# Kernel tuning notes

Measured on AMD Instinct MI355X. Metric: run time of the kernel, lower is better.

The kernel has to match this reference:

```python
import jax, jax.numpy as jnp
import numpy as np

B, N, K = 4, 1024, 20
DM, DI, DS, DC, DR = 1024, 2048, 16, 4, 64
BITS, GRID = 10, 0.02
BINS = (1, 2, 4, 8, 16, 32)


def _lrelu(x):
    return jnp.where(x >= 0, x, 0.2 * x)


def _bn(x, w, b, m, v, eps=1e-5):
    return (x - m) * (w * jax.lax.rsqrt(v + eps)) + b


def _ln(x, w, b, eps=1e-5):
    mu = jnp.mean(x, -1, keepdims=True)
    var = jnp.mean((x - mu) ** 2, -1, keepdims=True)
    return (x - mu) * jax.lax.rsqrt(var + eps) * w + b


def _knn(x, k):
    # x: (B,N,C) -> (B,N,k) indices of k nearest (largest neg sq dist)
    xx = jnp.sum(x * x, -1)
    d = 2 * jnp.einsum('bnc,bmc->bnm', x, x) - xx[:, :, None] - xx[:, None, :]
    return jax.lax.top_k(d, k)[1]


def _edge_conv(x, w, bw, bb, bm, bv, k):
    idx = _knn(x, k)
    nb = jax.vmap(lambda f, i: f[i])(x, idx)            # (B,N,k,C) row gather
    ctr = jnp.broadcast_to(x[:, :, None, :], nb.shape)
    feat = jnp.concatenate([nb - ctr, ctr], -1)         # (B,N,k,2C)
    h = _lrelu(_bn(jnp.einsum('bnkc,oc->bnko', feat, w), bw, bb, bm, bv))
    return jnp.max(h, axis=2)                           # (B,N,O)


def _hilbert(g):
    # Skilling's AxesToTranspose, 3D, BITS bits/axis. g: (...,3) int32 -> (...,) int32
    xs = [g[..., i] for i in range(3)]
    Q = 1 << (BITS - 1)
    while Q > 1:
        P = Q - 1
        for i in range(3):
            cond = (xs[i] & Q) != 0
            if i == 0:
                xs[0] = jnp.where(cond, xs[0] ^ P, xs[0])
            else:
                t = (xs[0] ^ xs[i]) & P
                n0 = jnp.where(cond, xs[0] ^ P, xs[0] ^ t)
                ni = jnp.where(cond, xs[i], xs[i] ^ t)
                xs[0], xs[i] = n0, ni
        Q >>= 1
    for i in range(1, 3):
        xs[i] = xs[i] ^ xs[i - 1]
    t = jnp.zeros_like(xs[0])
    Q = 1 << (BITS - 1)
    while Q > 1:
        t = jnp.where((xs[2] & Q) != 0, t ^ (Q - 1), t)
        Q >>= 1
    xs = [v ^ t for v in xs]
    code = jnp.zeros_like(xs[0])
    for bit in range(BITS - 1, -1, -1):
        for i in range(3):
            code = (code << 1) | ((xs[i] >> bit) & 1)
    return code


def _serial_order(pts, trans):
    g = jnp.floor(pts / GRID).astype(jnp.int32)
    g = g - jnp.min(g, axis=1, keepdims=True)
    g = jnp.clip(g, 0, (1 << BITS) - 1)
    if trans:
        g = g[..., jnp.array([1, 0, 2])]
    return jnp.argsort(_hilbert(g), axis=1)             # per-batch serialization order


def _take(f, o):
    return jnp.take_along_axis(f, o[..., None], axis=1)


def _mamba(x, in_w, conv_w, conv_b, xproj_w, dt_w, dt_b, A_log, Dp, out_w):
    Bm, L, _ = x.shape
    xc, z = jnp.split(x @ in_w.T, 2, axis=-1)           # (B,L,DI) each
    xp = jnp.pad(xc, ((0, 0), (DC - 1, 0), (0, 0)))     # causal depthwise conv
    xc = sum(conv_w[:, j] * xp[:, j:j + L, :] for j in range(DC)) + conv_b
    xc = jax.nn.silu(xc)
    xdbl = xc @ xproj_w.T
    dt, Bs, Cs = jnp.split(xdbl, [DR, DR + DS], axis=-1)
    dt = jax.nn.softplus(dt @ dt_w.T + dt_b)            # (B,L,DI)
    A = -jnp.exp(A_log)                                 # (DI,DS)

    def step(h, inp):
        dt_t, B_t, C_t, u_t = inp
        h = h * jnp.exp(dt_t[..., None] * A) + (dt_t * u_t)[..., None] * B_t[:, None, :]
        return h, jnp.einsum('bdn,bn->bd', h, C_t)

    tm = lambda a: jnp.moveaxis(a, 1, 0)
    h0 = jnp.zeros((Bm, DI, DS), x.dtype)
    _, ys = jax.lax.scan(step, h0, (tm(dt), tm(Bs), tm(Cs), tm(xc)))
    y = jnp.moveaxis(ys, 0, 1) + xc * Dp
    return (y * jax.nn.silu(z)) @ out_w.T


def _forward(x, c1_w, bn1_w, bn1_b, bn1_m, bn1_v, c2_w, bn2_w, bn2_b, bn2_m, bn2_v,
             c3_w, bn3_w, bn3_b, bn3_m, bn3_v, c4_w, bn4_w, bn4_b, bn4_m, bn4_v,
             c5_w, bn5_w, bn5_b, bn5_m, bn5_v, pe1_w, pe1_b, pe2_w, pe2_b,
             gamma, beta, blkn_w, blkn_b, in_w, conv_w, conv_b, xproj_w,
             dt_w, dt_b, A_log, D, out_w, normf_w, normf_b, ft_w, ft_b):
    pts = jnp.transpose(x, (0, 2, 1))                   # (B,N,3)
    x1 = _edge_conv(pts, c1_w, bn1_w, bn1_b, bn1_m, bn1_v, K)
    x2 = _edge_conv(x1, c2_w, bn2_w, bn2_b, bn2_m, bn2_v, K)
    x3 = _edge_conv(x2, c3_w, bn3_w, bn3_b, bn3_m, bn3_v, K)
    x4 = _edge_conv(x3, c4_w, bn4_w, bn4_b, bn4_m, bn4_v, K)
    dg = _lrelu(_bn(jnp.einsum('bnc,oc->bno', jnp.concatenate([x1, x2, x3, x4], -1), c5_w),
                    bn5_w, bn5_b, bn5_m, bn5_v))        # (B,N,1024)
    pos5 = jax.nn.gelu(pts @ pe1_w.T + pe1_b, approximate=False) @ pe2_w.T + pe2_b
    of = _serial_order(pts, False)
    ob = _serial_order(pts, True)
    xs = jnp.concatenate([_take(dg, of) * gamma + beta,
                          _take(dg, ob) * gamma + beta], 1)   # (B,2N,1024)
    ps = jnp.concatenate([_take(pos5, of), _take(pos5, ob)], 1)
    hs = xs + ps
    hs = hs + _mamba(_ln(hs, blkn_w, blkn_b), in_w, conv_w, conv_b, xproj_w,
                     dt_w, dt_b, A_log, D, out_w)
    hs = _ln(hs, normf_w, normf_b)
    x_all = jnp.concatenate([hs, dg], axis=1)           # (B,3N,1024)
    P = x_all.shape[1]
    feats = []
    for nbin in BINS:
        zz = x_all.reshape(B, nbin, P // nbin, DM)
        feats.append(jnp.mean(zz, 2) + jnp.max(zz, 2))
    bf = jnp.transpose(jnp.concatenate(feats, 1), (1, 0, 2))  # (63,B,1024)
    return bf @ ft_w.T + ft_b                           # (63,B,256)


def setup_inputs() -> dict:
    ks = iter(jax.random.split(jax.random.key(0), 80))
    f32 = jnp.float32
    def nrm(shape, s):
        return jax.random.normal(next(ks), shape, f32) * s
    d = {}
    d['x'] = jax.random.normal(next(ks), (B, 3, N), f32)
    for name, (o, i) in dict(c1=(64, 6), c2=(64, 128), c3=(128, 128),
                             c4=(256, 256), c5=(1024, 512)).items():
        d[name + '_w'] = nrm((o, i), 1.0 / np.sqrt(i))
    for name, c in dict(bn1=64, bn2=64, bn3=128, bn4=256, bn5=1024).items():
        d[name + '_w'] = 1.0 + nrm((c,), 0.05)
        d[name + '_b'] = nrm((c,), 0.05)
        d[name + '_m'] = nrm((c,), 0.05)
        d[name + '_v'] = 1.0 + 0.1 * jax.random.uniform(next(ks), (c,), f32)
    d['pe1_w'] = nrm((DM // 2, 3), 1.0 / np.sqrt(3))
    d['pe1_b'] = nrm((DM // 2,), 0.02)
    d['pe2_w'] = nrm((DM, DM // 2), 1.0 / np.sqrt(DM // 2))
    d['pe2_b'] = nrm((DM,), 0.02)
    d['gamma'] = 1.0 + nrm((DM,), 0.02)
    d['beta'] = nrm((DM,), 0.02)
    d['blkn_w'] = jnp.ones((DM,), f32)
    d['blkn_b'] = jnp.zeros((DM,), f32)
    d['in_w'] = nrm((2 * DI, DM), 1.0 / np.sqrt(DM))
    d['conv_w'] = nrm((DI, DC), 1.0 / np.sqrt(DC))
    d['conv_b'] = jnp.zeros((DI,), f32)
    d['xproj_w'] = nrm((DR + 2 * DS, DI), 1.0 / np.sqrt(DI))
    d['dt_w'] = nrm((DI, DR), DR ** -0.5)
    dt = jnp.exp(jax.random.uniform(next(ks), (DI,), f32) * np.log(0.1 / 1e-3) + np.log(1e-3))
    d['dt_b'] = dt + jnp.log(-jnp.expm1(-dt))           # inverse softplus
    d['A_log'] = jnp.log(jnp.broadcast_to(jnp.arange(1, DS + 1, dtype=f32), (DI, DS)))
    d['D'] = jnp.ones((DI,), f32)
    d['out_w'] = nrm((DM, DI), 1.0 / np.sqrt(DI))
    d['normf_w'] = jnp.ones((DM,), f32)
    d['normf_b'] = jnp.zeros((DM,), f32)
    d['ft_w'] = nrm((256, DM), 1.0 / np.sqrt(DM))
    d['ft_b'] = jnp.zeros((256,), f32)
    return d


def reference(x, c1_w, bn1_w, bn1_b, bn1_m, bn1_v, c2_w, bn2_w, bn2_b, bn2_m, bn2_v,
              c3_w, bn3_w, bn3_b, bn3_m, bn3_v, c4_w, bn4_w, bn4_b, bn4_m, bn4_v,
              c5_w, bn5_w, bn5_b, bn5_m, bn5_v, pe1_w, pe1_b, pe2_w, pe2_b,
              gamma, beta, blkn_w, blkn_b, in_w, conv_w, conv_b, xproj_w,
              dt_w, dt_b, A_log, D, out_w, normf_w, normf_b, ft_w, ft_b):
    return _forward(x, c1_w, bn1_w, bn1_b, bn1_m, bn1_v, c2_w, bn2_w, bn2_b, bn2_m, bn2_v,
                    c3_w, bn3_w, bn3_b, bn3_m, bn3_v, c4_w, bn4_w, bn4_b, bn4_m, bn4_v,
                    c5_w, bn5_w, bn5_b, bn5_m, bn5_v, pe1_w, pe1_b, pe2_w, pe2_b,
                    gamma, beta, blkn_w, blkn_b, in_w, conv_w, conv_b, xproj_w,
                    dt_w, dt_b, A_log, D, out_w, normf_w, normf_b, ft_w, ft_b)
```

## Files before the change

### kernel.cpp

```cpp
#include <hip/hip_runtime.h>
#include <hip/hip_bf16.h>
#include <cstdint>
#include <cstddef>

static constexpr int BB = 4, NN = 1024;
static constexpr int DM = 1024, DI = 2048, DSN = 16, DCN = 4;
static constexpr int LL = 2048, PP = 3072;

typedef unsigned short u16;
typedef __bf16 bfv8 __attribute__((ext_vector_type(8)));
typedef float fv4 __attribute__((ext_vector_type(4)));

__device__ __forceinline__ u16 f2bf(float f) {
  unsigned u = __float_as_uint(f);
  return (u16)((u + 0x7FFFu + ((u >> 16) & 1u)) >> 16);
}
__device__ __forceinline__ float bf2f(u16 h) { return __uint_as_float(((unsigned)h) << 16); }

__device__ __forceinline__ void gload_lds16(const void* g, void* l) {
  __builtin_amdgcn_global_load_lds((const __attribute__((address_space(1))) void*)g,
                                   (__attribute__((address_space(3))) void*)l, 16, 0, 0);
}

__global__ __launch_bounds__(256) void k_fill(unsigned* __restrict__ p, unsigned n32, unsigned pat) {
  unsigned i = blockIdx.x * 256 + threadIdx.x;
  if (i < n32) p[i] = pat;
}

struct CvtArgs {
  const void* src[47];
  unsigned dstoff[47];
  unsigned nelem[47];
  unsigned cumblk[48];
};

__global__ __launch_bounds__(256) void k_convert(CvtArgs a, float* __restrict__ ws) {
  const unsigned w0 = *(const unsigned*)a.src[32];
  const bool isbf = (w0 != 0x3F800000u);
  const int blk = (int)blockIdx.x;
  int slot = 46;
  while (slot > 0 && blk < (int)a.cumblk[slot]) --slot;
  const unsigned n = a.nelem[slot];
  const unsigned base = (unsigned)(blk - (int)a.cumblk[slot]) * 1024u + threadIdx.x;
  float* dst = ws + a.dstoff[slot];
  if (isbf) {
    const u16* s = (const u16*)a.src[slot];
#pragma unroll
    for (int p = 0; p < 4; ++p) {
      unsigned e = base + 256u * p;
      if (e < n) dst[e] = bf2f(s[e]);
    }
  } else {
    const float* s = (const float*)a.src[slot];
#pragma unroll
    for (int p = 0; p < 4; ++p) {
      unsigned e = base + 256u * p;
      if (e < n) dst[e] = s[e];
    }
  }
}

__global__ __launch_bounds__(256) void k_tobf(const float* __restrict__ s, u16* __restrict__ d, int n4) {
  int i = blockIdx.x * 256 + threadIdx.x;
  if (i >= n4) return;
  float4 v = *(const float4*)(s + (size_t)i * 4);
  uint2 o;
  o.x = (unsigned)f2bf(v.x) | ((unsigned)f2bf(v.y) << 16);
  o.y = (unsigned)f2bf(v.z) | ((unsigned)f2bf(v.w) << 16);
  *(uint2*)(d + (size_t)i * 4) = o;
}

__global__ __launch_bounds__(256) void k_transpose(const float* __restrict__ x, float* __restrict__ pts) {
  int o = blockIdx.x * 256 + threadIdx.x;
  if (o >= BB * NN * 3) return;
  int c = o % 3, n = (o / 3) % NN, b = o / (3 * NN);
  pts[o] = x[((size_t)b * 3 + c) * NN + n];
}

__global__ __launch_bounds__(256) void k_rownorm(const float* __restrict__ X, int ldx, int C, float* __restrict__ xx) {
  int r = blockIdx.x * 256 + threadIdx.x;
  if (r >= BB * NN) return;
  const float* p = X + (size_t)r * ldx;
  float s0 = 0, s1 = 0, s2 = 0, s3 = 0;
  int c = 0;
  for (; c + 4 <= C; c += 4) {
    s0 += p[c] * p[c]; s1 += p[c + 1] * p[c + 1];
    s2 += p[c + 2] * p[c + 2]; s3 += p[c + 3] * p[c + 3];
  }
  for (; c < C; ++c) s0 += p[c] * p[c];
  xx[r] = (s0 + s1) + (s2 + s3);
}

__global__ __launch_bounds__(256) void k_dist(const float* __restrict__ X, int ldx, int C,
                                              const float* __restrict__ xx, float* __restrict__ D) {
  const int b = blockIdx.z;
  const float* Xb = X + (size_t)(b << 10) * ldx;
  __shared__ float As[16][68];
  __shared__ float Bs[16][68];
  const int tid = threadIdx.x;
  const int m0 = blockIdx.y << 6, n0 = blockIdx.x << 6;
  const int tcol = tid & 15, trow = tid >> 4;
  float acc[4][4];
#pragma unroll
  for (int i = 0; i < 4; ++i)
#pragma unroll
    for (int j = 0; j < 4; ++j) acc[i][j] = 0.f;

  for (int k0 = 0; k0 < C; k0 += 16) {
#pragma unroll
    for (int p = 0; p < 4; ++p) {
      int lin = tid + (p << 8);
      int r = lin >> 4, kk = lin & 15;
      int gk = k0 + kk;
      As[kk][r] = (gk < C) ? Xb[(size_t)(m0 + r) * ldx + gk] : 0.f;
      Bs[kk][r] = (gk < C) ? Xb[(size_t)(n0 + r) * ldx + gk] : 0.f;
    }
    __syncthreads();
#pragma unroll
    for (int kk = 0; kk < 16; ++kk) {
      float a[4], bv[4];
#pragma unroll
      for (int i = 0; i < 4; ++i) a[i] = As[kk][(trow << 2) + i];
#pragma unroll
      for (int j = 0; j < 4; ++j) bv[j] = Bs[kk][(tcol << 2) + j];
#pragma unroll
      for (int i = 0; i < 4; ++i)
#pragma unroll
        for (int j = 0; j < 4; ++j) acc[i][j] += a[i] * bv[j];
    }
    __syncthreads();
  }

#pragma unroll
  for (int i = 0; i < 4; ++i) {
    int gm = m0 + (trow << 2) + i;
#pragma unroll
    for (int j = 0; j < 4; ++j) {
      int gn = n0 + (tcol << 2) + j;
      float v = 2.f * acc[i][j] - xx[(b << 10) + gm] - xx[(b << 10) + gn];
      D[((size_t)(b << 10) + gm) * 1024 + gn] = v;
    }
  }
}

__global__ __launch_bounds__(256) void k_sel(const float* __restrict__ D, int* __restrict__ idxo) {
  const int wv = threadIdx.x >> 6, lane = threadIdx.x & 63;
  const int row = (blockIdx.x << 2) + wv;
  const float* dr = D + (size_t)row * 1024;
  float4 c0 = *(const float4*)(dr + (lane << 2));
  float4 c1 = *(const float4*)(dr + 256 + (lane << 2));
  float4 c2 = *(const float4*)(dr + 512 + (lane << 2));
  float4 c3 = *(const float4*)(dr + 768 + (lane << 2));
  float v[16] = {c0.x, c0.y, c0.z, c0.w, c1.x, c1.y, c1.z, c1.w,
                 c2.x, c2.y, c2.z, c2.w, c3.x, c3.y, c3.z, c3.w};
  const int gbase = lane << 2;
  for (int t = 0; t < 20; ++t) {
    float bv = v[0];
    int bi = gbase;
#pragma unroll
    for (int r = 1; r < 16; ++r) {
      int gi = ((r >> 2) << 8) + gbase + (r & 3);
      if (v[r] > bv) { bv = v[r]; bi = gi; }
    }
#pragma unroll
    for (int o = 32; o; o >>= 1) {
      float ov = __shfl_down(bv, o);
      int oi = __shfl_down(bi, o);
      if (ov > bv || (ov == bv && oi < bi)) { bv = ov; bi = oi; }
    }
    bi = __shfl(bi, 0);
    if (lane == 0) idxo[row * 20 + t] = bi;
#pragma unroll
    for (int r = 0; r < 16; ++r) {
      int gi = ((r >> 2) << 8) + gbase + (r & 3);
      if (gi == bi) v[r] = -3e38f;
    }
  }
}

template <int O>
__global__ __launch_bounds__(256) void k_edge_max(const float* __restrict__ G, const float* __restrict__ base,
                                                  const int* __restrict__ idxi,
                                                  const float* __restrict__ bw, const float* __restrict__ bbp,
                                                  const float* __restrict__ bm, const float* __restrict__ bvv,
                                                  float* __restrict__ out, int ldo) {
  __shared__ int ids[20];
  const int rn = blockIdx.x;
  const int tid = threadIdx.x;
  if (tid < 20) ids[tid] = idxi[rn * 20 + tid];
  __syncthreads();
  const int b = rn >> 10;
  float mx = -3e38f, mn = 3e38f;
#pragma unroll 5
  for (int k = 0; k < 20; ++k) {
    float v = G[((size_t)(b << 10) + ids[k]) * O + tid];
    mx = fmaxf(mx, v); mn = fminf(mn, v);
  }
  float s = bw[tid] * rsqrtf(bvv[tid] + 1e-5f);
  float red = (s >= 0.f) ? mx : mn;
  float v = (base[(size_t)rn * O + tid] + red - bm[tid]) * s + bbp[tid];
  out[(size_t)rn * ldo + tid] = (v >= 0.f) ? v : 0.2f * v;
}

template <int EPI>
__global__ __launch_bounds__(256) void k_gemm(const float* __restrict__ A, int lda,
                                              const float* __restrict__ Bm, int ldb, int boff, int bdiff,
                                              float* __restrict__ C, int ldc, int M, int N, int Kd,
                                              const float* __restrict__ p1) {
  __shared__ float As[16][68];
  __shared__ float Bs[16][68];
  const int tid = threadIdx.x;
  const int m0 = blockIdx.y << 6, n0 = blockIdx.x << 6;
  const int tcol = tid & 15, trow = tid >> 4;
  float acc[4][4];
#pragma unroll
  for (int i = 0; i < 4; ++i)
#pragma unroll
    for (int j = 0; j < 4; ++j) acc[i][j] = 0.f;

  for (int k0 = 0; k0 < Kd; k0 += 16) {
#pragma unroll
    for (int p = 0; p < 4; ++p) {
      int lin = tid + (p << 8);
      int r = lin >> 4, kk = lin & 15;
      int gk = k0 + kk;
      int gm = m0 + r;
      As[kk][r] = (gm < M && gk < Kd) ? A[(size_t)gm * lda + gk] : 0.f;
      int gn = n0 + r;
      float bv = 0.f;
      if (gn < N && gk < Kd) {
        bv = Bm[(size_t)gn * ldb + gk + boff];
        if (bdiff) bv -= Bm[(size_t)gn * ldb + gk];
      }
      Bs[kk][r] = bv;
    }
    __syncthreads();
#pragma unroll
    for (int kk = 0; kk < 16; ++kk) {
      float a[4], bv[4];
#pragma unroll
      for (int i = 0; i < 4; ++i) a[i] = As[kk][(trow << 2) + i];
#pragma unroll
      for (int j = 0; j < 4; ++j) bv[j] = Bs[kk][(tcol << 2) + j];
#pragma unroll
      for (int i = 0; i < 4; ++i)
#pragma unroll
        for (int j = 0; j < 4; ++j) acc[i][j] += a[i] * bv[j];
    }
    __syncthreads();
  }

#pragma unroll
  for (int i = 0; i < 4; ++i) {
    int gm = m0 + (trow << 2) + i;
    if (gm >= M) continue;
#pragma unroll
    for (int j = 0; j < 4; ++j) {
      int gn = n0 + (tcol << 2) + j;
      if (gn >= N) continue;
      float v = acc[i][j];
      if (EPI == 2) {
        v += p1[gn];
        v = 0.5f * v * (1.f + erff(v * 0.70710678118654752440f));
      }
      C[(size_t)gm * ldc + gn] = v;
    }
  }
}

template <int EPI>
__global__ __launch_bounds__(256) void k_mgemm3(const u16* __restrict__ A, const u16* __restrict__ W,
                                                float* __restrict__ C, int ldc, int M, int N, int K, int alda,
                                                const float* __restrict__ p1, const float* __restrict__ p2,
                                                const float* __restrict__ p3, const float* __restrict__ p4,
                                                u16* __restrict__ obf, void* outp, const void* modesrc) {
  __shared__ char raw[65536];
  u16* Asl = (u16*)raw;
  u16* Bsl = (u16*)(raw + 32768);
  const int tid = threadIdx.x;
  const int lane = tid & 63, wave = tid >> 6;
  const int wm = wave & 1, wn = wave >> 1;
  const int m0 = blockIdx.y << 7, n0 = blockIdx.x << 7;
  fv4 acc[4][4];
#pragma unroll
  for (int i = 0; i < 4; ++i)
#pragma unroll
    for (int j = 0; j < 4; ++j) acc[i][j] = fv4{0.f, 0.f, 0.f, 0.f};

  const int lrow = tid >> 2;
  const int lcol = (((tid & 3) ^ ((tid >> 3) & 3)) << 3);
  const u16* gA0 = A + (size_t)(m0 + lrow) * alda + lcol;
  const u16* gA1 = A + (size_t)(m0 + 64 + lrow) * alda + lcol;
  const u16* gB0 = W + (size_t)(n0 + lrow) * K + lcol;
  const u16* gB1 = W + (size_t)(n0 + 64 + lrow) * K + lcol;
  const int ar = wm * 64 + (lane & 15);
  const int br = wn * 64 + (lane & 15);
  const int swz = ((lane & 15) >> 1) & 3;
  const int ko = (((lane >> 4) ^ swz) << 3);

  const int NIT = K >> 5;
#pragma unroll
  for (int p = 0; p < 2; ++p) {
    const int k0 = p << 5;
    gload_lds16(gA0 + k0, Asl + p * 4096 + wave * 512);
    gload_lds16(gA1 + k0, Asl + p * 4096 + 2048 + wave * 512);
    gload_lds16(gB0 + k0, Bsl + p * 4096 + wave * 512);
    gload_lds16(gB1 + k0, Bsl + p * 4096 + 2048 + wave * 512);
  }

  for (int it = 0; it < NIT; ++it) {
    if (it + 2 < NIT) {
      const int nb = (it + 2) & 3;
      const int k0 = (it + 2) << 5;
      gload_lds16(gA0 + k0, Asl + nb * 4096 + wave * 512);
      gload_lds16(gA1 + k0, Asl + nb * 4096 + 2048 + wave * 512);
      gload_lds16(gB0 + k0, Bsl + nb * 4096 + wave * 512);
      gload_lds16(gB1 + k0, Bsl + nb * 4096 + 2048 + wave * 512);
      asm volatile("s_waitcnt vmcnt(8)" ::: "memory");
    } else if (it + 1 < NIT) {
      asm volatile("s_waitcnt vmcnt(4)" ::: "memory");
    } else {
      asm volatile("s_waitcnt vmcnt(0)" ::: "memory");
    }
    __builtin_amdgcn_sched_barrier(0);
    __builtin_amdgcn_s_barrier();
    const int cb = it & 3;
    bfv8 af[4], bfr[4];
#pragma unroll
    for (int f = 0; f < 4; ++f) {
      af[f]  = *(const bfv8*)(Asl + cb * 4096 + (ar + f * 16) * 32 + ko);
      bfr[f] = *(const bfv8*)(Bsl + cb * 4096 + (br + f * 16) * 32 + ko);
    }
#pragma unroll
    for (int i = 0; i < 4; ++i)
#pragma unroll
      for (int j = 0; j < 4; ++j)
        acc[i][j] = __builtin_amdgcn_mfma_f32_16x16x32_bf16(af[i], bfr[j], acc[i][j], 0, 0, 0);
  }

  const int rq = lane >> 4, cq = lane & 15;
  if constexpr (EPI == 6) {
    bool isbf = (*(const unsigned*)modesrc) != 0x3F800000u;
#pragma unroll
    for (int i = 0; i < 4; ++i)
#pragma unroll
      for (int j = 0; j < 4; ++j)
#pragma unroll
        for (int r = 0; r < 4; ++r) {
          int gm = m0 + wm * 64 + i * 16 + rq * 4 + r;
          int gn = n0 + wn * 64 + j * 16 + cq;
          if (gm >= M || gn >= N) continue;
          float v = acc[i][j][r] + p1[gn];
          if (isbf) ((u16*)outp)[(size_t)gm * ldc + gn] = f2bf(v);
          else ((float*)outp)[(size_t)gm * ldc + gn] = v;
        }
  } else {
    constexpr bool U16O = (EPI == 1 || EPI == 8 || EPI == 9);
    __syncthreads();
#pragma unroll
    for (int i = 0; i < 4; ++i)
#pragma unroll
      for (int j = 0; j < 4; ++j)
#pragma unroll
        for (int r = 0; r < 4; ++r) {
          int row = wm * 64 + i * 16 + rq * 4 + r;
          int col = wn * 64 + j * 16 + cq;
          int gn = n0 + col;
          float v = acc[i][j][r];
          if (EPI == 1) {
            float s = p1[gn] * rsqrtf(p4[gn] + 1e-5f);
            v = (v - p3[gn]) * s + p2[gn];
            v = (v >= 0.f) ? v : 0.2f * v;
          } else if (EPI == 3) {
            v += p1[gn];
          } else if (EPI == 9) {
            v += p1[gn];
            v = (v > 0.f) ? v + __logf(1.f + __expf(-v)) : __logf(1.f + __expf(v));
          }
          int sc = col ^ ((row & 7) << 3);
          if (U16O) ((u16*)raw)[row * 128 + sc] = f2bf(v);
          else ((float*)raw)[row * 128 + sc] = v;
        }
    __syncthreads();
    const int row = tid >> 1, c0 = (tid & 1) << 6;
    const int gm = m0 + row;
    if (gm < M) {
      if (n0 + 128 <= N) {
        if (U16O) {
          u16* dst = obf + (size_t)gm * ldc + n0 + c0;
#pragma unroll
          for (int vv = 0; vv < 8; ++vv) {
            int sc = (c0 + vv * 8) ^ ((row & 7) << 3);
            *(uint4*)(dst + vv * 8) = *(const uint4*)((const u16*)raw + row * 128 + sc);
          }
        } else {
          float* dst = C + (size_t)gm * ldc + n0 + c0;
#pragma unroll
          for (int vv = 0; vv < 16; ++vv) {
            int sc = (c0 + vv * 4) ^ ((row & 7) << 3);
            float4 val = *(const float4*)((const float*)raw + row * 128 + sc);
            if (EPI == 5) {
              float4 o = *(const float4*)(dst + vv * 4);
              val.x += o.x; val.y += o.y; val.z += o.z; val.w += o.w;
            }
            *(float4*)(dst + vv * 4) = val;
          }
        }
      } else {
        for (int e = 0; e < 64; ++e) {
          int col = c0 + e, gn = n0 + col;
          if (gn >= N) break;
          int sc = col ^ ((row & 7) << 3);
          if (U16O) {
            obf[(size_t)gm * ldc + gn] = ((const u16*)raw)[row * 128 + sc];
          } else {
            float v = ((const float*)raw)[row * 128 + sc];
            if (EPI == 5) v += C[(size_t)gm * ldc + gn];
            C[(size_t)gm * ldc + gn] = v;
          }
        }
      }
    }
  }
}

__device__ __forceinline__ int hilbert3(int x0, int x1, int x2) {
  for (int Q = 1 << 9; Q > 1; Q >>= 1) {
    int P2 = Q - 1;
    if (x0 & Q) x0 ^= P2;
    { int t = (x0 ^ x1) & P2; if (x1 & Q) x0 ^= P2; else { x0 ^= t; x1 ^= t; } }
    { int t = (x0 ^ x2) & P2; if (x2 & Q) x0 ^= P2; else { x0 ^= t; x2 ^= t; } }
  }
  x1 ^= x0; x2 ^= x1;
  int t = 0;
  for (int Q = 1 << 9; Q > 1; Q >>= 1)
    if (x2 & Q) t ^= (Q - 1);
  x0 ^= t; x1 ^= t; x2 ^= t;
  int code = 0;
  for (int bit = 9; bit >= 0; --bit) {
    code = (code << 1) | ((x0 >> bit) & 1);
    code = (code << 1) | ((x1 >> bit) & 1);
    code = (code << 1) | ((x2 >> bit) & 1);
  }
  return code;
}

__global__ __launch_bounds__(1024) void k_serial(const float* __restrict__ pts, int* __restrict__ of, int* __restrict__ ob) {
  const int b = blockIdx.x >> 1, trans = blockIdx.x & 1;
  const int tid = threadIdx.x;
  __shared__ int mn[3];
  __shared__ unsigned long long sk[1024];
  if (tid < 3) mn[tid] = 0x7fffffff;
  __syncthreads();
  int g[3];
#pragma unroll
  for (int c = 0; c < 3; ++c) {
    float p = pts[((size_t)b * NN + tid) * 3 + c];
    g[c] = (int)floorf(p / 0.02f);
    atomicMin(&mn[c], g[c]);
  }
  __syncthreads();
#pragma unroll
  for (int c = 0; c < 3; ++c) {
    g[c] -= mn[c];
    g[c] = g[c] < 0 ? 0 : (g[c] > 1023 ? 1023 : g[c]);
  }
  int x0 = g[0], x1 = g[1], x2 = g[2];
  if (trans) { int t = x0; x0 = x1; x1 = t; }
  int code = hilbert3(x0, x1, x2);
  sk[tid] = ((unsigned long long)(unsigned)code << 10) | (unsigned)tid;
  __syncthreads();
  for (int k2 = 2; k2 <= 1024; k2 <<= 1) {
    for (int j = k2 >> 1; j > 0; j >>= 1) {
      int ixj = tid ^ j;
      if (ixj > tid) {
        unsigned long long a0 = sk[tid], a1 = sk[ixj];
        bool up = ((tid & k2) == 0);
        if ((a0 > a1) == up) { sk[tid] = a1; sk[ixj] = a0; }
      }
      __syncthreads();
    }
  }
  int* dst = trans ? ob : of;
  dst[b * NN + tid] = (int)(sk[tid] & 1023u);
}

__global__ __launch_bounds__(256) void k_build_hs(const u16* __restrict__ dg, const float* __restrict__ pos5,
                                                  const int* __restrict__ of, const int* __restrict__ ob,
                                                  const float* __restrict__ gamma, const float* __restrict__ beta,
                                                  float* __restrict__ hs) {
  const int row = blockIdx.x;
  const int b = row >> 11, l = row & 2047;
  const int src = (l < NN) ? of[b * NN + l] : ob[b * NN + (l - NN)];
  const u16* dgr = dg + ((size_t)b * NN + src) * DM;
  const float* psr = pos5 + ((size_t)b * NN + src) * DM;
  float* hr = hs + (size_t)row * DM;
  for (int c = threadIdx.x; c < DM; c += 256)
    hr[c] = bf2f(dgr[c]) * gamma[c] + beta[c] + psr[c];
}

__device__ __forceinline__ float wred_sum(float s) {
#pragma unroll
  for (int o = 32; o; o >>= 1) s += __shfl_down(s, o);
  return s;
}

template <int BF>
__global__ __launch_bounds__(256) void k_ln(const float* X, const float* __restrict__ w,
                                            const float* __restrict__ bb, float* Y, u16* Ybf) {
  const int row = blockIdx.x;
  const float* x = X + (size_t)row * DM;
  const int tid = threadIdx.x;
  float v[4];
#pragma unroll
  for (int p = 0; p < 4; ++p) v[p] = x[tid + (p << 8)];
  __shared__ float red[4];
  float s = ((v[0] + v[1]) + (v[2] + v[3]));
  s = wred_sum(s);
  if ((tid & 63) == 0) red[tid >> 6] = s;
  __syncthreads();
  float mu = (red[0] + red[1] + red[2] + red[3]) * (1.f / DM);
  __syncthreads();
  float ss = 0.f;
#pragma unroll
  for (int p = 0; p < 4; ++p) { float d = v[p] - mu; ss += d * d; }
  ss = wred_sum(ss);
  if ((tid & 63) == 0) red[tid >> 6] = ss;
  __syncthreads();
  float var = (red[0] + red[1] + red[2] + red[3]) * (1.f / DM);
  float rs = rsqrtf(var + 1e-5f);
#pragma unroll
  for (int p = 0; p < 4; ++p) {
    int c = tid + (p << 8);
    float o = (v[p] - mu) * rs * w[c] + bb[c];
    if (BF) Ybf[(size_t)row * DM + c] = f2bf(o);
    else Y[(size_t)row * DM + c] = o;
  }
}

__global__ __launch_bounds__(512) void k_convip(float* __restrict__ x, const float* __restrict__ cw,
                                                const float* __restrict__ cb, u16* __restrict__ xbf) {
  const int b = blockIdx.x >> 5, dgp = blockIdx.x & 31;
  const int lane = threadIdx.x & 63, ch = threadIdx.x >> 6;
  const int d = (dgp << 6) + lane;
  float* base = x + ((size_t)b * LL) * DI + d;
  u16* bb16 = xbf + ((size_t)b * LL) * DI + d;
  const int CL = LL / 8;
  const int l0 = ch * CL;
  const float w0 = cw[d * 4], w1 = cw[d * 4 + 1], w2 = cw[d * 4 + 2], w3 = cw[d * 4 + 3];
  const float bbv = cb[d];
  float a = 0.f, e = 0.f, c = 0.f;
  if (ch) {
    a = base[(size_t)(l0 - 3) * DI];
    e = base[(size_t)(l0 - 2) * DI];
    c = base[(size_t)(l0 - 1) * DI];
  }
  __syncthreads();
  for (int l = l0; l < l0 + CL; ++l) {
    float cur = base[(size_t)l * DI];
    float acc = bbv + w0 * a + w1 * e + w2 * c + w3 * cur;
    a = e; e = c; c = cur;
    float o = acc / (1.f + expf(-acc));
    base[(size_t)l * DI] = o;
    bb16[(size_t)l * DI] = f2bf(o);
  }
}

__global__ __launch_bounds__(64) void k_scanA_f(float* __restrict__ xy, const float* __restrict__ xdbl,
                                                const float* __restrict__ dtw, const float* __restrict__ dtbv,
                                                const float* __restrict__ A_log, const float* __restrict__ Dp,
                                                float* __restrict__ hend, float* __restrict__ dts,
                                                u16* __restrict__ zone) {
  const int t = threadIdx.x;
  const int seg = blockIdx.x & 15;
  const int dgrp = (blockIdx.x >> 4) & 31;
  const int b = blockIdx.x >> 9;
  const int d = (dgrp << 6) + t;
  const bool gate = (seg == 0);
  float wdt[64];
#pragma unroll
  for (int k = 0; k < 64; ++k) wdt[k] = dtw[d * 64 + k];
  float aa[16], h[16];
#pragma unroll
  for (int n = 0; n < 16; ++n) {
    aa[n] = -expf(A_log[d * 16 + n]) * 1.44269504088896340736f;
    h[n] = 0.f;
  }
  const float Dd = Dp[d], bdt = dtbv[d];
  const int l0 = seg << 7;
  float* base = xy + ((size_t)(b * LL + l0)) * DI + d;
  u16* zb = zone + ((size_t)(b * LL + l0)) * DI + d;
  const float* xr = xdbl + (size_t)(b * LL + l0) * 96;

  __shared__ float sx[2][768];
#pragma unroll
  for (int p = 0; p < 3; ++p)
    *(float4*)&sx[0][(t + (p << 6)) << 2] = *(const float4*)(xr + ((t + (p << 6)) << 2));
  float ureg[8], zreg[8];
#pragma unroll
  for (int r = 0; r < 8; ++r) ureg[r] = base[(size_t)r * DI];
  if (gate) {
#pragma unroll
    for (int r = 0; r < 8; ++r) zreg[r] = bf2f(zb[(size_t)r * DI]);
  }
  __syncthreads();

  float dta = 0.f;
  for (int lc = 0; lc < 16; ++lc) {
    const int cur = lc & 1;
    const bool more = (lc + 1 < 16);
    float4 st0, st1, st2;
    float unext[8], znext[8];
    if (more) {
      const float* src = xr + (size_t)(lc + 1) * 768;
      st0 = *(const float4*)(src + (t << 2));
      st1 = *(const float4*)(src + ((t + 64) << 2));
      st2 = *(const float4*)(src + ((t + 128) << 2));
#pragma unroll
      for (int r = 0; r < 8; ++r) unext[r] = base[(size_t)((lc + 1) * 8 + r) * DI];
      if (gate) {
#pragma unroll
        for (int r = 0; r < 8; ++r) znext[r] = bf2f(zb[(size_t)((lc + 1) * 8 + r) * DI]);
      }
    }
    float yv[8];
#pragma unroll
    for (int r = 0; r < 8; ++r) {
      const float* row = &sx[cur][r * 96];
      float s0 = 0, s1 = 0, s2 = 0, s3 = 0;
#pragma unroll
      for (int k = 0; k < 64; k += 4) {
        s0 += wdt[k] * row[k];     s1 += wdt[k + 1] * row[k + 1];
        s2 += wdt[k + 2] * row[k + 2]; s3 += wdt[k + 3] * row[k + 3];
      }
      float dv = (s0 + s1) + (s2 + s3) + bdt;
      dv = (dv > 0.f) ? dv + log1pf(expf(-dv)) : log1pf(expf(dv));
      dta += dv;
      float u = ureg[r];
      float du = dv * u;
      float acc = 0.f;
#pragma unroll
      for (int n = 0; n < 16; ++n) {
        float ee = exp2f(dv * aa[n]);
        h[n] = h[n] * ee + du * row[64 + n];
        acc += h[n] * row[80 + n];
      }
      yv[r] = acc + u * Dd;
    }
    if (gate) {
#pragma unroll
      for (int r = 0; r < 8; ++r) {
        float zv = zreg[r];
        zb[(size_t)(lc * 8 + r) * DI] = f2bf(yv[r] * (zv / (1.f + expf(-zv))));
      }
    } else {
#pragma unroll
      for (int r = 0; r < 8; ++r) base[(size_t)(lc * 8 + r) * DI] = yv[r];
    }
    __syncthreads();
    if (more) {
      *(float4*)&sx[cur ^ 1][t << 2] = st0;
      *(float4*)&sx[cur ^ 1][(t + 64) << 2] = st1;
      *(float4*)&sx[cur ^ 1][(t + 128) << 2] = st2;
#pragma unroll
      for (int r = 0; r < 8; ++r) ureg[r] = unext[r];
      if (gate) {
#pragma unroll
        for (int r = 0; r < 8; ++r) zreg[r] = znext[r];
      }
    }
    __syncthreads();
  }
  float* he = hend + ((size_t)(b * 16 + seg) * 16) * DI + d;
#pragma unroll
  for (int n = 0; n < 16; ++n) he[(size_t)n * DI] = h[n];
  dts[(size_t)(b * 16 + seg) * DI + d] = dta;
}

__global__ __launch_bounds__(64) void k_scanC_f(const float* __restrict__ xy, const float* __restrict__ xdbl,
                                                const float* __restrict__ dtw, const float* __restrict__ dtbv,
                                                const float* __restrict__ A_log,
                                                const float* __restrict__ hstart, u16* __restrict__ zone) {
  const int t = threadIdx.x;
  const int seg = (blockIdx.x % 15) + 1;
  const int rest = blockIdx.x / 15;
  const int dgrp = rest & 31;
  const int b = rest >> 5;
  const int d = (dgrp << 6) + t;
  float wdt[64];
#pragma unroll
  for (int k = 0; k < 64; ++k) wdt[k] = dtw[d * 64 + k];
  float aa[16], hst[16];
#pragma unroll
  for (int n = 0; n < 16; ++n) {
    aa[n] = -expf(A_log[d * 16 + n]) * 1.44269504088896340736f;
    hst[n] = hstart[((size_t)(b * 16 + seg) * 16 + n) * DI + d];
  }
  const float bdt = dtbv[d];
  const int l0 = seg << 7;
  const float* base = xy + ((size_t)(b * LL + l0)) * DI + d;
  u16* zb = zone + ((size_t)(b * LL + l0)) * DI + d;
  const float* xr = xdbl + (size_t)(b * LL + l0) * 96;

  __shared__ float sx[2][768];
#pragma unroll
  for (int p = 0; p < 3; ++p)
    *(float4*)&sx[0][(t + (p << 6)) << 2] = *(const float4*)(xr + ((t + (p << 6)) << 2));
  float ureg[8], zreg[8];
#pragma unroll
  for (int r = 0; r < 8; ++r) {
    ureg[r] = base[(size_t)r * DI];
    zreg[r] = bf2f(zb[(size_t)r * DI]);
  }
  __syncthreads();

  float cumdt = 0.f;
  for (int lc = 0; lc < 16; ++lc) {
    const int cur = lc & 1;
    const bool more = (lc + 1 < 16);
    float4 st0, st1, st2;
    float unext[8], znext[8];
    if (more) {
      const float* src = xr + (size_t)(lc + 1) * 768;
      st0 = *(const float4*)(src + (t << 2));
      st1 = *(const float4*)(src + ((t + 64) << 2));
      st2 = *(const float4*)(src + ((t + 128) << 2));
#pragma unroll
      for (int r = 0; r < 8; ++r) {
        unext[r] = base[(size_t)((lc + 1) * 8 + r) * DI];
        znext[r] = bf2f(zb[(size_t)((lc + 1) * 8 + r) * DI]);
      }
    }
    float yv[8];
#pragma unroll
    for (int r = 0; r < 8; ++r) {
      const float* row = &sx[cur][r * 96];
      float s0 = 0, s1 = 0, s2 = 0, s3 = 0;
#pragma unroll
      for (int k = 0; k < 64; k += 4) {
        s0 += wdt[k] * row[k];     s1 += wdt[k + 1] * row[k + 1];
        s2 += wdt[k + 2] * row[k + 2]; s3 += wdt[k + 3] * row[k + 3];
      }
      float dv = (s0 + s1) + (s2 + s3) + bdt;
      dv = (dv > 0.f) ? dv + log1pf(expf(-dv)) : log1pf(expf(dv));
      cumdt += dv;
      float corr = 0.f;
#pragma unroll
      for (int n = 0; n < 16; ++n)
        corr += row[80 + n] * exp2f(aa[n] * cumdt) * hst[n];
      yv[r] = ureg[r] + corr;
    }
#pragma unroll
    for (int r = 0; r < 8; ++r) {
      float zv = zreg[r];
      zb[(size_t)(lc * 8 + r) * DI] = f2bf(yv[r] * (zv / (1.f + expf(-zv))));
    }
    __syncthreads();
    if (more) {
      *(float4*)&sx[cur ^ 1][t << 2] = st0;
      *(float4*)&sx[cur ^ 1][(t + 64) << 2] = st1;
      *(float4*)&sx[cur ^ 1][(t + 128) << 2] = st2;
#pragma unroll
      for (int r = 0; r < 8; ++r) { ureg[r] = unext[r]; zreg[r] = znext[r]; }
    }
    __syncthreads();
  }
}

__global__ __launch_bounds__(64) void k_scanA_p(float* __restrict__ xy, const float* __restrict__ xdbl,
                                                const u16* __restrict__ dtb,
                                                const float* __restrict__ A_log, const float* __restrict__ Dp,
                                                float* __restrict__ hend, float* __restrict__ dts,
                                                u16* __restrict__ zone) {
  const int t = threadIdx.x;
  const int seg = blockIdx.x & 31;
  const int dgrp = (blockIdx.x >> 5) & 31;
  const int b = blockIdx.x >> 10;
  const int d = (dgrp << 6) + t;
  const bool gate = (seg == 0);
  float aa[16], h[16];
#pragma unroll
  for (int n = 0; n < 16; ++n) {
    aa[n] = -expf(A_log[d * 16 + n]) * 1.44269504088896340736f;
    h[n] = 0.f;
  }
  const float Dd = Dp[d];
  const int l0 = seg << 6;
  float* base = xy + ((size_t)(b * LL + l0)) * DI + d;
  const u16* dtp = dtb + ((size_t)(b * LL + l0)) * DI + d;
  u16* zb = zone + ((size_t)(b * LL + l0)) * DI + d;
  const float* xr = xdbl + (size_t)(b * LL + l0) * 96 + 64;

  __shared__ float sx[2][256];
  const int sr = t >> 3, sq = (t & 7) << 2;
  *(float4*)&sx[0][sr * 32 + sq] = *(const float4*)(xr + sr * 96 + sq);
  float ureg[8], dreg[8], zreg[8];
#pragma unroll
  for (int r = 0; r < 8; ++r) { ureg[r] = base[(size_t)r * DI]; dreg[r] = bf2f(dtp[(size_t)r * DI]); }
  if (gate) {
#pragma unroll
    for (int r = 0; r < 8; ++r) zreg[r] = bf2f(zb[(size_t)r * DI]);
  }
  __syncthreads();

  float dta = 0.f;
  for (int lc = 0; lc < 8; ++lc) {
    const int cur = lc & 1;
    const bool more = (lc + 1 < 8);
    float4 st0;
    float unext[8], dnext[8], znext[8];
    if (more) {
      st0 = *(const float4*)(xr + (size_t)(lc + 1) * 768 + sr * 96 + sq);
#pragma unroll
      for (int r = 0; r < 8; ++r) {
        unext[r] = base[(size_t)((lc + 1) * 8 + r) * DI];
        dnext[r] = bf2f(dtp[(size_t)((lc + 1) * 8 + r) * DI]);
      }
      if (gate) {
#pragma unroll
        for (int r = 0; r < 8; ++r) znext[r] = bf2f(zb[(size_t)((lc + 1) * 8 + r) * DI]);
      }
    }
    float yv[8];
#pragma unroll
    for (int r = 0; r < 8; ++r) {
      const float* row = &sx[cur][r * 32];
      float dv = dreg[r];
      dta += dv;
      float u = ureg[r];
      float du = dv * u;
      float acc = 0.f;
#pragma unroll
      for (int n = 0; n < 16; ++n) {
        float ee = exp2f(dv * aa[n]);
        h[n] = h[n] * ee + du * row[n];
        acc += h[n] * row[16 + n];
      }
      yv[r] = acc + u * Dd;
    }
    if (gate) {
#pragma unroll
      for (int r = 0; r < 8; ++r) {
        float zv = zreg[r];
        zb[(size_t)(lc * 8 + r) * DI] = f2bf(yv[r] * (zv / (1.f + expf(-zv))));
      }
    } else {
#pragma unroll
      for (int r = 0; r < 8; ++r) base[(size_t)(lc * 8 + r) * DI] = yv[r];
    }
    __syncthreads();
    if (more) {
      *(float4*)&sx[cur ^ 1][sr * 32 + sq] = st0;
#pragma unroll
      for (int r = 0; r < 8; ++r) { ureg[r] = unext[r]; dreg[r] = dnext[r]; }
      if (gate) {
#pragma unroll
        for (int r = 0; r < 8; ++r) zreg[r] = znext[r];
      }
    }
    __syncthreads();
  }
  float* he = hend + ((size_t)(b * 32 + seg) * 16) * DI + d;
#pragma unroll
  for (int n = 0; n < 16; ++n) he[(size_t)n * DI] = h[n];
  dts[(size_t)(b * 32 + seg) * DI + d] = dta;
}

__global__ __launch_bounds__(64) void k_scanC_p(const float* __restrict__ xy, const float* __restrict__ xdbl,
                                                const u16* __restrict__ dtb,
                                                const float* __restrict__ A_log,
                                                const float* __restrict__ hstart, u16* __restrict__ zone) {
  const int t = threadIdx.x;
  const int seg = (blockIdx.x % 31) + 1;
  const int rest = blockIdx.x / 31;
  const int dgrp = rest & 31;
  const int b = rest >> 5;
  const int d = (dgrp << 6) + t;
  float aa[16], hst[16];
#pragma unroll
  for (int n = 0; n < 16; ++n) {
    aa[n] = -expf(A_log[d * 16 + n]) * 1.44269504088896340736f;
    hst[n] = hstart[((size_t)(b * 32 + seg) * 16 + n) * DI + d];
  }
  const int l0 = seg << 6;
  const float* base = xy + ((size_t)(b * LL + l0)) * DI + d;
  const u16* dtp = dtb + ((size_t)(b * LL + l0)) * DI + d;
  u16* zb = zone + ((size_t)(b * LL + l0)) * DI + d;
  const float* xr = xdbl + (size_t)(b * LL + l0) * 96 + 64;

  __shared__ float sx[2][256];
  const int sr = t >> 3, sq = (t & 7) << 2;
  *(float4*)&sx[0][sr * 32 + sq] = *(const float4*)(xr + sr * 96 + sq);
  float ureg[8], dreg[8], zreg[8];
#pragma unroll
  for (int r = 0; r < 8; ++r) {
    ureg[r] = base[(size_t)r * DI];
    dreg[r] = bf2f(dtp[(size_t)r * DI]);
    zreg[r] = bf2f(zb[(size_t)r * DI]);
  }
  __syncthreads();

  float cumdt = 0.f;
  for (int lc = 0; lc < 8; ++lc) {
    const int cur = lc & 1;
    const bool more = (lc + 1 < 8);
    float4 st0;
    float unext[8], dnext[8], znext[8];
    if (more) {
      st0 = *(const float4*)(xr + (size_t)(lc + 1) * 768 + sr * 96 + sq);
#pragma unroll
      for (int r = 0; r < 8; ++r) {
        unext[r] = base[(size_t)((lc + 1) * 8 + r) * DI];
        dnext[r] = bf2f(dtp[(size_t)((lc + 1) * 8 + r) * DI]);
        znext[r] = bf2f(zb[(size_t)((lc + 1) * 8 + r) * DI]);
      }
    }
    float yv[8];
#pragma unroll
    for (int r = 0; r < 8; ++r) {
      const float* row = &sx[cur][r * 32];
      cumdt += dreg[r];
      float corr = 0.f;
#pragma unroll
      for (int n = 0; n < 16; ++n)
        corr += row[16 + n] * exp2f(aa[n] * cumdt) * hst[n];
      yv[r] = ureg[r] + corr;
    }
#pragma unroll
    for (int r = 0; r < 8; ++r) {
      float zv = zreg[r];
      zb[(size_t)(lc * 8 + r) * DI] = f2bf(yv[r] * (zv / (1.f + expf(-zv))));
    }
    __syncthreads();
    if (more) {
      *(float4*)&sx[cur ^ 1][sr * 32 + sq] = st0;
#pragma unroll
      for (int r = 0; r < 8; ++r) { ureg[r] = unext[r]; dreg[r] = dnext[r]; zreg[r] = znext[r]; }
    }
    __syncthreads();
  }
}

__global__ __launch_bounds__(256) void k_scanB(float* __restrict__ hh, const float* __restrict__ dts,
                                               const float* __restrict__ A_log, int nseg) {
  const int i = blockIdx.x * 256 + threadIdx.x;
  const int b = i >> 11, d = i & 2047;
  float aa[16], hs_[16];
#pragma unroll
  for (int n = 0; n < 16; ++n) {
    aa[n] = -expf(A_log[d * 16 + n]) * 1.44269504088896340736f;
    hs_[n] = 0.f;
  }
  for (int s = 0; s < nseg; ++s) {
    float* p = hh + ((size_t)(b * nseg + s) * 16) * DI + d;
    const float ds = dts[(size_t)(b * nseg + s) * DI + d];
#pragma unroll
    for (int n = 0; n < 16; ++n) {
      float he = p[(size_t)n * DI];
      p[(size_t)n * DI] = hs_[n];
      hs_[n] = he + exp2f(aa[n] * ds) * hs_[n];
    }
  }
}

__global__ __launch_bounds__(256) void k_binpool1(const float* __restrict__ hs, const u16* __restrict__ dg,
                                                  float* __restrict__ psum, float* __restrict__ pmax) {
  const int blk = blockIdx.x;
  const int cg = blk & 3, chunk = (blk >> 2) & 31, b = blk >> 7;
  const int c = (cg << 8) + threadIdx.x;
  const int r0 = chunk * 96;
  float sm = 0.f, mx = -3e38f;
  for (int r = 0; r < 96; ++r) {
    int pr = r0 + r;
    float v = (pr < 2048) ? hs[((size_t)(b << 11) + pr) * 1024 + c]
                          : bf2f(dg[((size_t)(b << 10) + (pr - 2048)) * 1024 + c]);
    sm += v; mx = fmaxf(mx, v);
  }
  int o = ((b << 5) + chunk) * 1024 + c;
  psum[o] = sm; pmax[o] = mx;
}

__global__ __launch_bounds__(256) void k_binpool2(const float* __restrict__ psum, const float* __restrict__ pmax,
                                                  float* __restrict__ bf) {
  const int sb = blockIdx.x;
  const int s = sb >> 2, b = sb & 3;
  int nbin, j;
  if (s == 0) { nbin = 1; j = 0; }
  else if (s < 3) { nbin = 2; j = s - 1; }
  else if (s < 7) { nbin = 4; j = s - 3; }
  else if (s < 15) { nbin = 8; j = s - 7; }
  else if (s < 31) { nbin = 16; j = s - 15; }
  else { nbin = 32; j = s - 31; }
  const int nch = 32 / nbin, c0 = j * nch;
  const int tid = threadIdx.x;
#pragma unroll
  for (int p = 0; p < 4; ++p) {
    int c = tid + (p << 8);
    float sm = 0.f, mx = -3e38f;
    for (int k = 0; k < nch; ++k) {
      int idx = ((b << 5) + c0 + k) * 1024 + c;
      sm += psum[idx]; mx = fmaxf(mx, pmax[idx]);
    }
    bf[(size_t)sb * 1024 + c] = sm / (float)(nch * 96) + mx;
  }
}

extern "C" void kernel_launch(void* const* d_in, const int* in_sizes, int n_in,
                              void* d_out, int out_size, void* d_ws, size_t ws_size,
                              hipStream_t stream) {
  const unsigned n32 = (unsigned)(out_size / 2);
  if (n_in != 47) {
    k_fill<<<(n32 + 255) / 256, 256, 0, stream>>>((unsigned*)d_out, n32, 0x44FA44FAu);
    return;
  }
  float* ws = (float*)d_ws;

  unsigned inoff[47];
  unsigned cum = 0;
  for (int i = 0; i < 47; ++i) { inoff[i] = cum; cum += (unsigned)((in_sizes[i] + 63) & ~63); }

  size_t off = ((size_t)cum + 255) & ~(size_t)255;
  auto alloc = [&](size_t nf) { size_t o = off; off = (off + nf + 255) & ~(size_t)255; return o; };
  const size_t O_DG = alloc(2097152);
  const size_t O_HS = alloc(8388608);
  const size_t O_B1 = alloc(16777216);
  const size_t O_B2 = alloc(6291456);
  const size_t O_B3 = alloc(12353536);
  const size_t base_end = off;
  const size_t O_DT = alloc(8388608);
  const size_t dt_end = off;
  if (base_end * 4 > ws_size) {
    k_fill<<<(n32 + 255) / 256, 256, 0, stream>>>((unsigned*)d_out, n32, 0x447A447Au);
    return;
  }
  const bool bigws = (dt_end * 4 <= ws_size);

  auto F = [&](int i) { return ws + inoff[i]; };
  u16*   dg_bf = (u16*)(ws + O_DG);
  float* hs = ws + O_HS;
  float* B1 = ws + O_B1;
  float* B2 = ws + O_B2;
  float* B3 = ws + O_B3;
  u16*   dtb_bf = (u16*)(ws + O_DT);

  float* pts   = B1;
  float* xxb   = B1 + 16384;
  int*   idxb  = (int*)(B1 + 32768);
  int*   of    = (int*)(B1 + 114688);
  int*   ob    = (int*)(B1 + 118784);
  float* xcat  = B1 + 131072;
  float* G     = B1 + 2228224;
  float* baseb = B1 + 3276800;
  float* tb    = B1 + 4325376;
  float* pos5  = B1 + 6422528;
  float* dist  = B1 + 10616832;
  u16*   xcat_bf = (u16*)(B1 + 12582912);
  u16*   tb_bf   = (u16*)(B1 + 14680064);
  float* xyg = B1;
  u16*   lnh_bf = (u16*)B2;
  float* hend   = B2;
  float* xdbl   = B2 + 4194304;
  float* bfb    = B2 + 4980736;
  u16*   bfb_bf = (u16*)(B2 + 5238784);
  float* psum   = B2 + 5369856;
  float* pmax   = B2 + 5500928;
  u16*   xdbl_bf = (u16*)(B2 + 5632000);
  float* dtsum  = psum;
  u16* in_w_bf  = (u16*)B3;
  u16* out_w_bf = (u16*)(B3 + 2097152);
  u16* c5_bf    = (u16*)(B3 + 3145728);
  u16* pe2_bf   = (u16*)(B3 + 3407872);
  u16* ft_bf    = (u16*)(B3 + 3670016);
  u16* xpw_bf   = (u16*)(B3 + 3801088);
  u16* dtw_bf   = (u16*)(B3 + 3899392);
  u16* zone     = (u16*)(B3 + 3964928);

  CvtArgs ca;
  unsigned cb = 0;
  for (int i = 0; i < 47; ++i) {
    ca.src[i] = d_in[i];
    ca.dstoff[i] = inoff[i];
    ca.nelem[i] = (unsigned)in_sizes[i];
    ca.cumblk[i] = cb;
    cb += (unsigned)((in_sizes[i] + 1023) / 1024);
  }
  ca.cumblk[47] = cb;
  k_convert<<<cb, 256, 0, stream>>>(ca, ws);

  k_tobf<<<4096, 256, 0, stream>>>(F(34), in_w_bf, 1048576);
  k_tobf<<<2048, 256, 0, stream>>>(F(42), out_w_bf, 524288);
  k_tobf<<<512, 256, 0, stream>>>(F(5), c5_bf, 131072);
  k_tobf<<<512, 256, 0, stream>>>(F(28), pe2_bf, 131072);
  k_tobf<<<256, 256, 0, stream>>>(F(45), ft_bf, 65536);
  k_tobf<<<192, 256, 0, stream>>>(F(37), xpw_bf, 49152);
  k_tobf<<<128, 256, 0, stream>>>(F(38), dtw_bf, 32768);

  k_transpose<<<(BB * NN * 3 + 255) / 256, 256, 0, stream>>>(F(0), pts);

  k_rownorm<<<16, 256, 0, stream>>>(pts, 3, 3, xxb);
  k_dist<<<dim3(16, 16, 4), 256, 0, stream>>>(pts, 3, 3, xxb, dist);
  k_sel<<<1024, 256, 0, stream>>>(dist, idxb);
  k_gemm<0><<<dim3(1, 64), 256, 0, stream>>>(pts, 3, F(1), 6, 0, 0, G, 64, 4096, 64, 3, nullptr);
  k_gemm<0><<<dim3(1, 64), 256, 0, stream>>>(pts, 3, F(1), 6, 3, 1, baseb, 64, 4096, 64, 3, nullptr);
  k_edge_max<64><<<4096, 64, 0, stream>>>(G, baseb, idxb, F(6), F(7), F(8), F(9), xcat + 0, 512);

  k_rownorm<<<16, 256, 0, stream>>>(xcat, 512, 64, xxb);
  k_dist<<<dim3(16, 16, 4), 256, 0, stream>>>(xcat, 512, 64, xxb, dist);
  k_sel<<<1024, 256, 0, stream>>>(dist, idxb);
  k_gemm<0><<<dim3(1, 64), 256, 0, stream>>>(xcat, 512, F(2), 128, 0, 0, G, 64, 4096, 64, 64, nullptr);
  k_gemm<0><<<dim3(1, 64), 256, 0, stream>>>(xcat, 512, F(2), 128, 64, 1, baseb, 64, 4096, 64, 64, nullptr);
  k_edge_max<64><<<4096, 64, 0, stream>>>(G, baseb, idxb, F(10), F(11), F(12), F(13), xcat + 64, 512);

  k_rownorm<<<16, 256, 0, stream>>>(xcat + 64, 512, 64, xxb);
  k_dist<<<dim3(16, 16, 4), 256, 0, stream>>>(xcat + 64, 512, 64, xxb, dist);
  k_sel<<<1024, 256, 0, stream>>>(dist, idxb);
  k_gemm<0><<<dim3(2, 64), 256, 0, stream>>>(xcat + 64, 512, F(3), 128, 0, 0, G, 128, 4096, 128, 64, nullptr);
  k_gemm<0><<<dim3(2, 64), 256, 0, stream>>>(xcat + 64, 512, F(3), 128, 64, 1, baseb, 128, 4096, 128, 64, nullptr);
  k_edge_max<128><<<4096, 128, 0, stream>>>(G, baseb, idxb, F(14), F(15), F(16), F(17), xcat + 128, 512);

  k_rownorm<<<16, 256, 0, stream>>>(xcat + 128, 512, 128, xxb);
  k_dist<<<dim3(16, 16, 4), 256, 0, stream>>>(xcat + 128, 512, 128, xxb, dist);
  k_sel<<<1024, 256, 0, stream>>>(dist, idxb);
  k_gemm<0><<<dim3(4, 64), 256, 0, stream>>>(xcat + 128, 512, F(4), 256, 0, 0, G, 256, 4096, 256, 128, nullptr);
  k_gemm<0><<<dim3(4, 64), 256, 0, stream>>>(xcat + 128, 512, F(4), 256, 128, 1, baseb, 256, 4096, 256, 128, nullptr);
  k_edge_max<256><<<4096, 256, 0, stream>>>(G, baseb, idxb, F(18), F(19), F(20), F(21), xcat + 256, 512);

  const float* np = nullptr;
  k_tobf<<<2048, 256, 0, stream>>>(xcat, xcat_bf, 524288);
  k_mgemm3<1><<<dim3(8, 32), 256, 0, stream>>>(xcat_bf, c5_bf, nullptr, 1024, 4096, 1024, 512, 512,
                                               F(22), F(23), F(24), F(25), dg_bf, nullptr, nullptr);

  k_gemm<2><<<dim3(8, 64), 256, 0, stream>>>(pts, 3, F(26), 3, 0, 0, tb, 512, 4096, 512, 3, F(27));
  k_tobf<<<2048, 256, 0, stream>>>(tb, tb_bf, 524288);
  k_mgemm3<3><<<dim3(8, 32), 256, 0, stream>>>(tb_bf, pe2_bf, pos5, 1024, 4096, 1024, 512, 512,
                                               F(29), np, np, np, nullptr, nullptr, nullptr);

  k_serial<<<8, 1024, 0, stream>>>(pts, of, ob);

  k_build_hs<<<8192, 256, 0, stream>>>(dg_bf, pos5, of, ob, F(30), F(31), hs);

  k_ln<1><<<8192, 256, 0, stream>>>(hs, F(32), F(33), nullptr, lnh_bf);
  k_mgemm3<0><<<dim3(16, 64), 256, 0, stream>>>(lnh_bf, in_w_bf, xyg, 2048, 8192, 2048, 1024, 1024,
                                                np, np, np, np, nullptr, nullptr, nullptr);
  k_convip<<<128, 512, 0, stream>>>(xyg, F(35), F(36), zone);
  k_mgemm3<0><<<dim3(1, 64), 256, 0, stream>>>(zone, xpw_bf, xdbl, 96, 8192, 96, 2048, 2048,
                                               np, np, np, np, nullptr, nullptr, nullptr);
  if (bigws) {
    k_tobf<<<768, 256, 0, stream>>>(xdbl, xdbl_bf, 196608);
    k_mgemm3<9><<<dim3(16, 64), 256, 0, stream>>>(xdbl_bf, dtw_bf, nullptr, 2048, 8192, 2048, 64, 96,
                                                  F(39), np, np, np, dtb_bf, nullptr, nullptr);
  }
  k_mgemm3<8><<<dim3(16, 64), 256, 0, stream>>>(lnh_bf, in_w_bf + 2097152, nullptr, 2048, 8192, 2048, 1024, 1024,
                                                np, np, np, np, zone, nullptr, nullptr);
  if (bigws) {
    k_scanA_p<<<4096, 64, 0, stream>>>(xyg, xdbl, dtb_bf, F(40), F(41), hend, dtsum, zone);
    k_scanB<<<32, 256, 0, stream>>>(hend, dtsum, F(40), 32);
    k_scanC_p<<<3968, 64, 0, stream>>>(xyg, xdbl, dtb_bf, F(40), hend, zone);
  } else {
    k_scanA_f<<<2048, 64, 0, stream>>>(xyg, xdbl, F(38), F(39), F(40), F(41), hend, dtsum, zone);
    k_scanB<<<32, 256, 0, stream>>>(hend, dtsum, F(40), 16);
    k_scanC_f<<<1920, 64, 0, stream>>>(xyg, xdbl, F(38), F(39), F(40), hend, zone);
  }
  k_mgemm3<5><<<dim3(8, 64), 256, 0, stream>>>(zone, out_w_bf, hs, 1024, 8192, 1024, 2048, 2048,
                                               np, np, np, np, nullptr, nullptr, nullptr);

  k_ln<0><<<8192, 256, 0, stream>>>(hs, F(43), F(44), hs, nullptr);

  k_binpool1<<<512, 256, 0, stream>>>(hs, dg_bf, psum, pmax);
  k_binpool2<<<252, 256, 0, stream>>>(psum, pmax, bfb);

  k_tobf<<<252, 256, 0, stream>>>(bfb, bfb_bf, 64512);
  k_mgemm3<6><<<dim3(2, 2), 256, 0, stream>>>(bfb_bf, ft_bf, nullptr, 256, 252, 256, 1024, 1024,
                                              F(46), np, np, np, nullptr, d_out, d_in[32]);
}
```

Baseline: 1.193 ms.

## Exploit distance symmetry in kNN and geometric A structure in scans

The distance kernel now computes only the lower-triangular tiles and writes each result to both (i,j) and (j,i), which roughly halves the GEMM work at the cost of transposed, uncoalesced stores. The three selective-scan kernels check at runtime whether A's rows form a geometric sequence (A[n] = (n+1)·A[0]). When they do, the 16 per-state exponentials become one exp2 followed by repeated multiplies, cutting transcendental work in the scan loops. The fallback path keeps general inputs correct, though the chained multiplies can accumulate rounding differences against the direct exponentials.

```diff
diff --git a/kernel.cpp b/kernel.cpp
--- a/kernel.cpp
+++ b/kernel.cpp
@@ -20,6 +20,14 @@
 __device__ __forceinline__ void gload_lds16(const void* g, void* l) {
   __builtin_amdgcn_global_load_lds((const __attribute__((address_space(1))) void*)g,
                                    (__attribute__((address_space(3))) void*)l, 16, 0, 0);
+}
+
+__device__ __forceinline__ bool geom_check(const float* aa) {
+  bool g = true;
+#pragma unroll
+  for (int n = 1; n < 16; ++n)
+    g = g && (fabsf(aa[n] - (float)(n + 1) * aa[0]) <= 1e-4f * fabsf(aa[n]) + 1e-12f);
+  return g;
 }
 
 __global__ __launch_bounds__(256) void k_fill(unsigned* __restrict__ p, unsigned n32, unsigned pat) {
@@ -93,6 +101,7 @@
 
 __global__ __launch_bounds__(256) void k_dist(const float* __restrict__ X, int ldx, int C,
                                               const float* __restrict__ xx, float* __restrict__ D) {
+  if (blockIdx.y < blockIdx.x) return;
   const int b = blockIdx.z;
   const float* Xb = X + (size_t)(b << 10) * ldx;
   __shared__ float As[16][68];
@@ -131,6 +140,7 @@
     __syncthreads();
   }
 
+  const bool diag = (m0 == n0);
 #pragma unroll
   for (int i = 0; i < 4; ++i) {
     int gm = m0 + (trow << 2) + i;
@@ -139,6 +149,7 @@
       int gn = n0 + (tcol << 2) + j;
       float v = 2.f * acc[i][j] - xx[(b << 10) + gm] - xx[(b << 10) + gn];
       D[((size_t)(b << 10) + gm) * 1024 + gn] = v;
+      if (!diag) D[((size_t)(b << 10) + gn) * 1024 + gm] = v;
     }
   }
 }
@@ -784,6 +795,7 @@
     aa[n] = -expf(A_log[d * 16 + n]) * 1.44269504088896340736f;
     h[n] = 0.f;
   }
+  const bool geom = geom_check(aa);
   const float Dd = Dp[d];
   const int l0 = seg << 6;
   float* base = xy + ((size_t)(b * LL + l0)) * DI + d;
@@ -829,11 +841,19 @@
       dta += dv;
       float u = ureg[r];
       float du = dv * u;
+      float es[16];
+      es[0] = exp2f(dv * aa[0]);
+      if (geom) {
+#pragma unroll
+        for (int n = 1; n < 16; ++n) es[n] = es[n - 1] * es[0];
+      } else {
+#pragma unroll
+        for (int n = 1; n < 16; ++n) es[n] = exp2f(dv * aa[n]);
+      }
       float acc = 0.f;
 #pragma unroll
       for (int n = 0; n < 16; ++n) {
-        float ee = exp2f(dv * aa[n]);
-        h[n] = h[n] * ee + du * row[n];
+        h[n] = h[n] * es[n] + du * row[n];
         acc += h[n] * row[16 + n];
       }
       yv[r] = acc + u * Dd;
@@ -882,6 +902,7 @@
     aa[n] = -expf(A_log[d * 16 + n]) * 1.44269504088896340736f;
     hst[n] = hstart[((size_t)(b * 32 + seg) * 16 + n) * DI + d];
   }
+  const bool geom = geom_check(aa);
   const int l0 = seg << 6;
   const float* base = xy + ((size_t)(b * LL + l0)) * DI + d;
   const u16* dtp = dtb + ((size_t)(b * LL + l0)) * DI + d;
@@ -920,10 +941,19 @@
     for (int r = 0; r < 8; ++r) {
       const float* row = &sx[cur][r * 32];
       cumdt += dreg[r];
+      float es[16];
+      es[0] = exp2f(aa[0] * cumdt);
+      if (geom) {
+#pragma unroll
+        for (int n = 1; n < 16; ++n) es[n] = es[n - 1] * es[0];
+      } else {
+#pragma unroll
+        for (int n = 1; n < 16; ++n) es[n] = exp2f(aa[n] * cumdt);
+      }
       float corr = 0.f;
 #pragma unroll
       for (int n = 0; n < 16; ++n)
-        corr += row[16 + n] * exp2f(aa[n] * cumdt) * hst[n];
+        corr += row[16 + n] * es[n] * hst[n];
       yv[r] = ureg[r] + corr;
     }
 #pragma unroll
@@ -951,14 +981,24 @@
     aa[n] = -expf(A_log[d * 16 + n]) * 1.44269504088896340736f;
     hs_[n] = 0.f;
   }
+  const bool geom = geom_check(aa);
   for (int s = 0; s < nseg; ++s) {
     float* p = hh + ((size_t)(b * nseg + s) * 16) * DI + d;
     const float ds = dts[(size_t)(b * nseg + s) * DI + d];
+    float es[16];
+    es[0] = exp2f(aa[0] * ds);
+    if (geom) {
+#pragma unroll
+      for (int n = 1; n < 16; ++n) es[n] = es[n - 1] * es[0];
+    } else {
+#pragma unroll
+      for (int n = 1; n < 16; ++n) es[n] = exp2f(aa[n] * ds);
+    }
 #pragma unroll
     for (int n = 0; n < 16; ++n) {
       float he = p[(size_t)n * DI];
       p[(size_t)n * DI] = hs_[n];
-      hs_[n] = he + exp2f(aa[n] * ds) * hs_[n];
+      hs_[n] = he + es[n] * hs_[n];
     }
   }
 }
```

New measurement: 1.291 ms. 8.2% more time.
